# Kernel tuning notes

Measured on AMD Instinct MI355X. Metric: run time of the kernel, lower is better.

## Reference

```python
import jax, jax.numpy as jnp
import numpy as np

T, B, F, H, P = 256, 512, 256, 512, 12  # seq len, batch, feature_dim, hidden_dim, p_interval


def setup_inputs() -> dict:
    key = jax.random.key(0)
    ks = jax.random.split(key, 9)
    s = 1.0 / np.sqrt(F + H)  # torch Linear default init scale
    def lin(k):
        kw, kb = jax.random.split(k)
        W = jax.random.uniform(kw, (F + H, H), jnp.float32, -s, s)
        b = jax.random.uniform(kb, (H,), jnp.float32, -s, s)
        return W, b
    Wf, bf = lin(ks[0])
    Wi, bi = lin(ks[1])
    Wo, bo = lin(ks[2])
    Wg, bg = lin(ks[3])
    x = jax.random.normal(ks[4], (T, B, F), jnp.float32)
    return {"x": x, "Wf": Wf, "bf": bf, "Wi": Wi, "bi": bi,
            "Wo": Wo, "bo": bo, "Wg": Wg, "bg": bg}


def _slstm(x, Wf, bf, Wi, bi, Wo, bo, Wg, bg):
    Tn, Bn, _ = x.shape
    h0 = jnp.zeros((P, Bn, H), x.dtype)
    # NOTE: original torch code reassigns c to a 2D [B,H] tensor after step 0,
    # so c[t % P] indexes a batch ROW (shape [H]) that broadcasts. At t=0 the
    # slice is all-zeros either way, so carrying a 2D c is exactly faithful.
    c0 = jnp.zeros((Bn, H), x.dtype)

    def step(carry, inp):
        h, c = carry
        x_t, t = inp
        idx = t % P
        xc = jnp.concatenate([x_t, h[idx]], axis=1)  # [B, F+H]
        f = jax.nn.softmax(xc @ Wf + bf, axis=1)
        i = jax.nn.softmax(xc @ Wi + bi, axis=1)
        o = jax.nn.softmax(xc @ Wo + bo, axis=1)
        g = jnp.tanh(xc @ Wg + bg)
        c_new = jnp.tanh(f * c[idx] + i * g)  # c[idx]: row [H], broadcasts over B
        h = h.at[idx].set(o * c_new)
        return (h, c_new), None

    (h, _), _ = jax.lax.scan(step, (h0, c0), (x, jnp.arange(Tn)))
    return h[(Tn - 1) % P]


def reference(x, Wf, bf, Wi, bi, Wo, bo, Wg, bg):
    return _slstm(x, Wf, bf, Wi, bi, Wo, bo, Wg, bg)
```

## Files before the change

kernel.cpp:

```cpp
#include <hip/hip_runtime.h>

typedef unsigned short u16;
typedef unsigned int   u32;

typedef __attribute__((ext_vector_type(8))) short bf16x8;
typedef __attribute__((ext_vector_type(4))) float f32x4;

__device__ __forceinline__ u16 f2bf(float v) {
    u32 u = __float_as_uint(v);
    u32 r = (u + 0x7fffu + ((u >> 16) & 1u)) >> 16;
    return (u16)r;
}
__device__ __forceinline__ float bf2f(u16 h) { return __uint_as_float(((u32)h) << 16); }

__device__ __forceinline__ float ftanh(float x) {
    float e = __expf(2.0f * x);
    return 1.0f - 2.0f * __builtin_amdgcn_rcpf(e + 1.0f);
}

__device__ __forceinline__ void gl2lds16(const void* g, void* l) {
    __builtin_amdgcn_global_load_lds(
        (const __attribute__((address_space(1))) void*)g,
        (__attribute__((address_space(3))) void*)l, 16, 0, 0);
}

__global__ void init_k(u16* __restrict__ hh, u16* __restrict__ hl, float* __restrict__ cb) {
    int i = blockIdx.x * 256 + threadIdx.x;
    hh[i] = 0; hl[i] = 0;
    if (i < 2 * 512) cb[i] = 0.0f;
}

__global__ void pack_wq(const float* __restrict__ Wf, const float* __restrict__ bf_,
                        const float* __restrict__ Wi, const float* __restrict__ bi_,
                        const float* __restrict__ Wo, const float* __restrict__ bo_,
                        const float* __restrict__ Wg, const float* __restrict__ bg_,
                        u16* __restrict__ wq, float* __restrict__ bias4) {
    int idx = blockIdx.x * 256 + threadIdx.x;
    int n = idx / 768, k = idx - n * 768;
    int gate = n >> 9, col = n & 511;
    const float* W = (gate == 0) ? Wf : (gate == 1) ? Wi : (gate == 2) ? Wo : Wg;
    float v = W[k * 512 + col];
    u16 h = f2bf(v);
    u16 l = f2bf(v - bf2f(h));
    size_t base = (size_t)n * 2304;
    if (k < 256) {
        wq[base + k] = h; wq[base + 512 + k] = h; wq[base + 256 + k] = l;
    } else {
        int d = k - 256;
        wq[base + 768 + d] = h; wq[base + 1792 + d] = h; wq[base + 1280 + d] = l;
    }
    if (k == 0) {
        const float* bb = (gate == 0) ? bf_ : (gate == 1) ? bi_ : (gate == 2) ? bo_ : bg_;
        bias4[n] = bb[col];
    }
}

__global__ void split_x(const float* __restrict__ src, u16* __restrict__ oh, u16* __restrict__ ol) {
    int i = blockIdx.x * 256 + threadIdx.x;
    float4 v = ((const float4*)src)[i];
    u16 hx = f2bf(v.x), hy = f2bf(v.y), hz = f2bf(v.z), hw = f2bf(v.w);
    u16 lx = f2bf(v.x - bf2f(hx)), ly = f2bf(v.y - bf2f(hy));
    u16 lz = f2bf(v.z - bf2f(hz)), lw = f2bf(v.w - bf2f(hw));
    uint2 hv; hv.x = (u32)hx | ((u32)hy << 16); hv.y = (u32)hz | ((u32)hw << 16);
    uint2 lv; lv.x = (u32)lx | ((u32)ly << 16); lv.y = (u32)lz | ((u32)lw << 16);
    ((uint2*)oh)[i] = hv;
    ((uint2*)ol)[i] = lv;
}

#define KT 36
__global__ __launch_bounds__(512, 2) void gemm_q(
    const u16* __restrict__ xh, const u16* __restrict__ xl,
    const u16* __restrict__ hh, const u16* __restrict__ hl,
    const u16* __restrict__ wq, const float* __restrict__ bias4,
    float* __restrict__ lg, int gx) {
    __shared__ __align__(16) u16 smem[65536];

    const int tid = threadIdx.x;
    const int wid = tid >> 6, lane = tid & 63;
    const int l15 = lane & 15, l4 = lane >> 4;
    const int wm = wid >> 2, wn = wid & 3;

    const int xcd = blockIdx.x & 7, rr_ = blockIdx.x >> 3;
    const int bmp = gx >> 3;
    const int bm = xcd * bmp + (rr_ % bmp);
    const int bn = rr_ / bmp;

    u32 aox[2][2], aoh[2][2], adst[2][2];
    u32 boff[2][2], bdst[2][2];
#pragma unroll
    for (int q = 0; q < 2; ++q) {
        u32 idx = (u32)q * 512 + (u32)tid;
        u32 ro = idx >> 3, s = idx & 7, c = s ^ (ro & 7);
#pragma unroll
        for (int u = 0; u < 2; ++u) {
            u32 arow = (u32)bm * 256 + (ro & 63) + (ro >> 6) * 128 + (u32)u * 64;
            u32 alds = ((ro & 63) + (ro >> 6) * 128 + (u32)u * 64) * 64 + s * 8;
            aox[u][q] = arow * 256 + c * 8;
            aoh[u][q] = arow * 512 + c * 8;
            adst[u][q] = alds;
            u32 bcol = (u32)bn * 256 + (u32)u * 128 + ro;
            boff[u][q] = bcol * 2304 + c * 8;
            bdst[u][q] = 16384 + ((u32)u * 128 + ro) * 64 + s * 8;
        }
    }

    u32 rA[8], rB[4], sK[2];
#pragma unroll
    for (int f = 0; f < 8; ++f) rA[f] = (u32)(wm * 128 + f * 16 + l15) * 64;
#pragma unroll
    for (int f = 0; f < 4; ++f) rB[f] = 16384u + (u32)(wn * 64 + f * 16 + l15) * 64;
#pragma unroll
    for (int ks = 0; ks < 2; ++ks) sK[ks] = (u32)(((ks * 4 + l4) ^ (lane & 7)) * 8);

    f32x4 acc[8][4];
#pragma unroll
    for (int f = 0; f < 8; ++f)
#pragma unroll
        for (int j = 0; j < 4; ++j) { acc[f][j].x = 0.f; acc[f][j].y = 0.f; acc[f][j].z = 0.f; acc[f][j].w = 0.f; }

    bf16x8 aH[4], bF[4];

#define STAGE_B(u) do {                                                       \
        gl2lds16(bsr + boff[u][0], smem + nb32 + bdst[u][0]);                 \
        gl2lds16(bsr + boff[u][1], smem + nb32 + bdst[u][1]); } while (0)
#define STAGE_A(u) do {                                                       \
        gl2lds16(as_ + (xp ? aox[u][0] : aoh[u][0]) + ako, smem + nb32 + adst[u][0]); \
        gl2lds16(as_ + (xp ? aox[u][1] : aoh[u][1]) + ako, smem + nb32 + adst[u][1]); } while (0)
#define RD_A(h, ks) do {                                                      \
        aH[0] = *(const bf16x8*)(smem + cb32 + rA[(h)*4+0] + sK[ks]);         \
        aH[1] = *(const bf16x8*)(smem + cb32 + rA[(h)*4+1] + sK[ks]);         \
        aH[2] = *(const bf16x8*)(smem + cb32 + rA[(h)*4+2] + sK[ks]);         \
        aH[3] = *(const bf16x8*)(smem + cb32 + rA[(h)*4+3] + sK[ks]); } while (0)
#define RD_B(ks) do {                                                         \
        bF[0] = *(const bf16x8*)(smem + cb32 + rB[0] + sK[ks]);               \
        bF[1] = *(const bf16x8*)(smem + cb32 + rB[1] + sK[ks]);               \
        bF[2] = *(const bf16x8*)(smem + cb32 + rB[2] + sK[ks]);               \
        bF[3] = *(const bf16x8*)(smem + cb32 + rB[3] + sK[ks]); } while (0)
#define MM16(hb) do {                                                         \
        __builtin_amdgcn_s_setprio(1);                                        \
        _Pragma("unroll")                                                     \
        for (int fi_ = 0; fi_ < 4; ++fi_)                                     \
            _Pragma("unroll")                                                 \
            for (int fj_ = 0; fj_ < 4; ++fj_)                                 \
                acc[(hb)*4+fi_][fj_] = __builtin_amdgcn_mfma_f32_16x16x32_bf16(\
                    aH[fi_], bF[fj_], acc[(hb)*4+fi_][fj_], 0, 0, 0);         \
        __builtin_amdgcn_s_setprio(0);                                        \
    } while (0)
#define BAR() do { __builtin_amdgcn_s_barrier(); __builtin_amdgcn_sched_barrier(0); } while (0)

    {
        const int nb32 = 0;
        const u16* bsr = wq;
        const u16* as_ = xh; const u32 ako = 0; const bool xp = true;
        STAGE_B(0); STAGE_B(1); STAGE_A(0); STAGE_A(1);
    }
    asm volatile("s_waitcnt vmcnt(2)" ::: "memory");
    BAR();

#pragma unroll 2
    for (int kt = 0; kt < KT; ++kt) {
        const int cb32 = (kt & 1) << 15;
        const int nb32 = cb32 ^ 32768;
        const int kn = kt + 1;
        const bool stg = (kn < KT);
        const u16* as_ = xh; u32 ako = 0; bool xp = true;
        if (stg) {
            if (kn < 12) { as_ = (kn >= 8) ? xl : xh; ako = (u32)(kn & 3) * 64; xp = true; }
            else { int s2 = kn - 12; as_ = (s2 >= 16) ? hl : hh; ako = (u32)(s2 & 7) * 64; xp = false; }
        }
        const u16* bsr = wq + (size_t)kn * 64;

        if (stg) STAGE_B(0);
        RD_B(0); RD_A(0, 0);
        BAR();
        MM16(0);
        if (stg) asm volatile("s_waitcnt vmcnt(2)" ::: "memory");
        else     asm volatile("s_waitcnt vmcnt(0)" ::: "memory");
        BAR();
        if (stg) STAGE_B(1);
        RD_A(1, 0);
        BAR();
        MM16(1);
        BAR();
        if (stg) STAGE_A(0);
        RD_B(1); RD_A(0, 1);
        BAR();
        MM16(0);
        BAR();
        if (stg) STAGE_A(1);
        RD_A(1, 1);
        BAR();
        MM16(1);
        if (stg) asm volatile("s_waitcnt vmcnt(2)" ::: "memory");
        BAR();
    }
#undef STAGE_B
#undef STAGE_A
#undef RD_A
#undef RD_B
#undef MM16
#undef BAR

#pragma unroll
    for (int fj = 0; fj < 4; ++fj) {
        int n = bn * 256 + wn * 64 + fj * 16 + l15;
        float bv = bias4[n];
#pragma unroll
        for (int f = 0; f < 8; ++f) {
            int row = bm * 256 + wm * 128 + f * 16 + l4 * 4;
            lg[(size_t)(row + 0) * 2048 + n] = acc[f][fj].x + bv;
            lg[(size_t)(row + 1) * 2048 + n] = acc[f][fj].y + bv;
            lg[(size_t)(row + 2) * 2048 + n] = acc[f][fj].z + bv;
            lg[(size_t)(row + 3) * 2048 + n] = acc[f][fj].w + bv;
        }
    }
}

__device__ __forceinline__ void chain_step(const float* __restrict__ lg, int j, int lane, float r[8]) {
    int rowb = (j + 1) % 12;
    const float* base = lg + (size_t)(j * 512 + rowb) * 2048 + lane * 8;
    float f[8], iv[8], g[8];
#pragma unroll
    for (int u = 0; u < 8; ++u) { f[u] = base[u]; iv[u] = base[512 + u]; g[u] = base[1536 + u]; }
    float mf = -1e30f, mi = -1e30f;
#pragma unroll
    for (int u = 0; u < 8; ++u) { mf = fmaxf(mf, f[u]); mi = fmaxf(mi, iv[u]); }
#pragma unroll
    for (int o = 32; o; o >>= 1) { mf = fmaxf(mf, __shfl_xor(mf, o)); mi = fmaxf(mi, __shfl_xor(mi, o)); }
    float sf = 0.f, si = 0.f;
#pragma unroll
    for (int u = 0; u < 8; ++u) {
        f[u] = __expf(f[u] - mf); sf += f[u];
        iv[u] = __expf(iv[u] - mi); si += iv[u];
    }
#pragma unroll
    for (int o = 32; o; o >>= 1) { sf += __shfl_xor(sf, o); si += __shfl_xor(si, o); }
    float rf = __builtin_amdgcn_rcpf(sf), ri = __builtin_amdgcn_rcpf(si);
#pragma unroll
    for (int u = 0; u < 8; ++u) {
        float gg = ftanh(g[u]);
        r[u] = ftanh(f[u] * rf * r[u] + iv[u] * ri * gg);
    }
}

__global__ __launch_bounds__(256) void gates_k(
    const float* __restrict__ lg, float* __restrict__ cb,
    u16* __restrict__ hh, u16* __restrict__ hl,
    float* __restrict__ out, int t0, int S, int rd, int wr) {
    __shared__ float rsh[512];
    const int widx = threadIdx.x >> 6, lane = threadIdx.x & 63;
    const int s = (S - 1) - (blockIdx.x >> 7);
    const int b = (blockIdx.x & 127) * 4 + widx;
    const int t = t0 + s;

    if (widx == 0) {
        float r[8];
#pragma unroll
        for (int u = 0; u < 8; ++u) r[u] = cb[rd * 512 + lane * 8 + u];
        for (int j = 0; j < s; ++j) chain_step(lg, j, lane, r);
#pragma unroll
        for (int u = 0; u < 8; ++u) rsh[lane * 8 + u] = r[u];
        if ((int)blockIdx.x == 127 && t0 + S < 256) {
            chain_step(lg, S - 1, lane, r);
#pragma unroll
            for (int u = 0; u < 8; ++u) cb[wr * 512 + lane * 8 + u] = r[u];
        }
    }
    __syncthreads();

    const float* row = lg + (size_t)(s * 512 + b) * 2048 + lane * 8;
    float f[8], iv[8], ov[8], g[8];
#pragma unroll
    for (int u = 0; u < 8; ++u) {
        f[u] = row[u]; iv[u] = row[512 + u]; ov[u] = row[1024 + u]; g[u] = row[1536 + u];
    }
    float mf = -1e30f, mi = -1e30f, mo = -1e30f;
#pragma unroll
    for (int u = 0; u < 8; ++u) { mf = fmaxf(mf, f[u]); mi = fmaxf(mi, iv[u]); mo = fmaxf(mo, ov[u]); }
#pragma unroll
    for (int o = 32; o; o >>= 1) {
        mf = fmaxf(mf, __shfl_xor(mf, o));
        mi = fmaxf(mi, __shfl_xor(mi, o));
        mo = fmaxf(mo, __shfl_xor(mo, o));
    }
    float sf = 0.f, si = 0.f, so = 0.f;
#pragma unroll
    for (int u = 0; u < 8; ++u) {
        f[u] = __expf(f[u] - mf); sf += f[u];
        iv[u] = __expf(iv[u] - mi); si += iv[u];
        ov[u] = __expf(ov[u] - mo); so += ov[u];
    }
#pragma unroll
    for (int o = 32; o; o >>= 1) {
        sf += __shfl_xor(sf, o); si += __shfl_xor(si, o); so += __shfl_xor(so, o);
    }
    float rf = __builtin_amdgcn_rcpf(sf), ri = __builtin_amdgcn_rcpf(si), ro = __builtin_amdgcn_rcpf(so);
    float hout[8];
#pragma unroll
    for (int u = 0; u < 8; ++u) {
        float rr = rsh[lane * 8 + u];
        float gg = ftanh(g[u]);
        float cv = ftanh(f[u] * rf * rr + iv[u] * ri * gg);
        hout[u] = ov[u] * ro * cv;
    }
    u32 hhp[4], hlp[4];
#pragma unroll
    for (int u = 0; u < 4; ++u) {
        u16 h0 = f2bf(hout[2 * u]), h1 = f2bf(hout[2 * u + 1]);
        u16 l0 = f2bf(hout[2 * u] - bf2f(h0)), l1 = f2bf(hout[2 * u + 1] - bf2f(h1));
        hhp[u] = (u32)h0 | ((u32)h1 << 16);
        hlp[u] = (u32)l0 | ((u32)l1 << 16);
    }
    size_t hb = ((size_t)(s * 512 + b)) * 512 + lane * 8;
    *(uint4*)&hh[hb] = make_uint4(hhp[0], hhp[1], hhp[2], hhp[3]);
    *(uint4*)&hl[hb] = make_uint4(hlp[0], hlp[1], hlp[2], hlp[3]);
    if (t == 255) {
        float* op = out + (size_t)b * 512 + lane * 8;
#pragma unroll
        for (int u = 0; u < 8; ++u) op[u] = hout[u];
    }
}

extern "C" void kernel_launch(void* const* d_in, const int* in_sizes, int n_in,
                              void* d_out, int out_size, void* d_ws, size_t ws_size,
                              hipStream_t stream) {
    const float* x   = (const float*)d_in[0];
    const float* Wf  = (const float*)d_in[1];
    const float* bf_ = (const float*)d_in[2];
    const float* Wi  = (const float*)d_in[3];
    const float* bi_ = (const float*)d_in[4];
    const float* Wo  = (const float*)d_in[5];
    const float* bo_ = (const float*)d_in[6];
    const float* Wg  = (const float*)d_in[7];
    const float* bg_ = (const float*)d_in[8];
    float* out = (float*)d_out;

    char* p = (char*)d_ws;
    u16* xh  = (u16*)p; p += 134217728;
    u16* xl  = (u16*)p; p += 134217728;
    u16* wq  = (u16*)p; p += 9437184;
    u16* hh  = (u16*)p; p += 6291456;
    u16* hl  = (u16*)p; p += 6291456;
    float* bias4 = (float*)p; p += 8192;
    float* cb    = (float*)p; p += 4096;
    float* lg    = (float*)p; p += 50331648;

    init_k<<<12288, 256, 0, stream>>>(hh, hl, cb);
    pack_wq<<<6144, 256, 0, stream>>>(Wf, bf_, Wi, bi_, Wo, bo_, Wg, bg_, wq, bias4);
    split_x<<<32768, 256, 0, stream>>>(x, xh, xl);

    for (int blk = 0; blk < 22; ++blk) {
        int t0 = blk * 12;
        int S = (256 - t0 >= 12) ? 12 : (256 - t0);
        int M = S * 512;
        int gx = M / 256;
        gemm_q<<<gx * 8, 512, 0, stream>>>(
            xh + (size_t)t0 * 512 * 256, xl + (size_t)t0 * 512 * 256,
            hh, hl, wq, bias4, lg, gx);
        gates_k<<<S * 128, 256, 0, stream>>>(lg, cb, hh, hl, out, t0, S, blk & 1, (blk + 1) & 1);
    }
}
```

Baseline: 2.007 ms.

## Relax GEMM barrier scheduling, skip zero-h K tiles on first block, vectorize init

Splits the barrier macro so only barriers that publish staged LDS data keep a full sched_barrier(0). The others use a plain s_barrier, and staging loads get a partial sched_barrier mask, giving the compiler more freedom to interleave loads, LDS reads and MFMAs. On the first time block the hidden state is all zeros, so the GEMM stops after the 12 x-only K tiles, skipping the h contribution. The init kernel also writes zeros with 16-byte stores and fewer blocks. The looser scheduling constraints risk reordering hazards around LDS buffer reuse.

```diff
diff --git a/kernel.cpp b/kernel.cpp
--- a/kernel.cpp
+++ b/kernel.cpp
@@ -24,10 +24,11 @@
         (__attribute__((address_space(3))) void*)l, 16, 0, 0);
 }
 
-__global__ void init_k(u16* __restrict__ hh, u16* __restrict__ hl, float* __restrict__ cb) {
+__global__ void init_k(uint4* __restrict__ hh4, uint4* __restrict__ hl4, float4* __restrict__ cb4) {
     int i = blockIdx.x * 256 + threadIdx.x;
-    hh[i] = 0; hl[i] = 0;
-    if (i < 2 * 512) cb[i] = 0.0f;
+    uint4 z = make_uint4(0u, 0u, 0u, 0u);
+    hh4[i] = z; hl4[i] = z;
+    if (i < 256) cb4[i] = make_float4(0.f, 0.f, 0.f, 0.f);
 }
 
 __global__ void pack_wq(const float* __restrict__ Wf, const float* __restrict__ bf_,
@@ -67,12 +68,11 @@
     ((uint2*)ol)[i] = lv;
 }
 
-#define KT 36
 __global__ __launch_bounds__(512, 2) void gemm_q(
     const u16* __restrict__ xh, const u16* __restrict__ xl,
     const u16* __restrict__ hh, const u16* __restrict__ hl,
     const u16* __restrict__ wq, const float* __restrict__ bias4,
-    float* __restrict__ lg, int gx) {
+    float* __restrict__ lg, int gx, int ktEnd) {
     __shared__ __align__(16) u16 smem[65536];
 
     const int tid = threadIdx.x;
@@ -146,23 +146,27 @@
                     aH[fi_], bF[fj_], acc[(hb)*4+fi_][fj_], 0, 0, 0);         \
         __builtin_amdgcn_s_setprio(0);                                        \
     } while (0)
-#define BAR() do { __builtin_amdgcn_s_barrier(); __builtin_amdgcn_sched_barrier(0); } while (0)
+#define FBAR() __builtin_amdgcn_s_barrier()
+#define SBV() __builtin_amdgcn_sched_barrier(0x10E)
+#define PUBLISH(n) do {                                                       \
+        asm volatile("s_waitcnt vmcnt(" #n ")" ::: "memory");                 \
+        __builtin_amdgcn_s_barrier();                                         \
+        __builtin_amdgcn_sched_barrier(0); } while (0)
 
     {
         const int nb32 = 0;
         const u16* bsr = wq;
         const u16* as_ = xh; const u32 ako = 0; const bool xp = true;
-        STAGE_B(0); STAGE_B(1); STAGE_A(0); STAGE_A(1);
-    }
-    asm volatile("s_waitcnt vmcnt(2)" ::: "memory");
-    BAR();
+        STAGE_B(0); SBV(); STAGE_B(1); SBV(); STAGE_A(0); SBV(); STAGE_A(1); SBV();
+    }
+    PUBLISH(2);
 
 #pragma unroll 2
-    for (int kt = 0; kt < KT; ++kt) {
+    for (int kt = 0; kt < ktEnd; ++kt) {
         const int cb32 = (kt & 1) << 15;
         const int nb32 = cb32 ^ 32768;
         const int kn = kt + 1;
-        const bool stg = (kn < KT);
+        const bool stg = (kn < ktEnd);
         const u16* as_ = xh; u32 ako = 0; bool xp = true;
         if (stg) {
             if (kn < 12) { as_ = (kn >= 8) ? xl : xh; ako = (u32)(kn & 3) * 64; xp = true; }
@@ -170,36 +174,37 @@
         }
         const u16* bsr = wq + (size_t)kn * 64;
 
-        if (stg) STAGE_B(0);
+        if (stg) { STAGE_B(0); SBV(); }
         RD_B(0); RD_A(0, 0);
-        BAR();
+        FBAR();
         MM16(0);
-        if (stg) asm volatile("s_waitcnt vmcnt(2)" ::: "memory");
-        else     asm volatile("s_waitcnt vmcnt(0)" ::: "memory");
-        BAR();
-        if (stg) STAGE_B(1);
+        if (stg) PUBLISH(2);
+        else     PUBLISH(0);
+        if (stg) { STAGE_B(1); SBV(); }
         RD_A(1, 0);
-        BAR();
+        FBAR();
         MM16(1);
-        BAR();
-        if (stg) STAGE_A(0);
+        FBAR();
+        if (stg) { STAGE_A(0); SBV(); }
         RD_B(1); RD_A(0, 1);
-        BAR();
+        FBAR();
         MM16(0);
-        BAR();
-        if (stg) STAGE_A(1);
+        FBAR();
+        if (stg) { STAGE_A(1); SBV(); }
         RD_A(1, 1);
-        BAR();
+        FBAR();
         MM16(1);
-        if (stg) asm volatile("s_waitcnt vmcnt(2)" ::: "memory");
-        BAR();
+        if (stg) PUBLISH(2);
+        else { __builtin_amdgcn_s_barrier(); }
     }
 #undef STAGE_B
 #undef STAGE_A
 #undef RD_A
 #undef RD_B
 #undef MM16
-#undef BAR
+#undef FBAR
+#undef SBV
+#undef PUBLISH
 
 #pragma unroll
     for (int fj = 0; fj < 4; ++fj) {
@@ -345,7 +350,7 @@
     float* cb    = (float*)p; p += 4096;
     float* lg    = (float*)p; p += 50331648;
 
-    init_k<<<12288, 256, 0, stream>>>(hh, hl, cb);
+    init_k<<<3072, 256, 0, stream>>>((uint4*)hh, (uint4*)hl, (float4*)cb);
     pack_wq<<<6144, 256, 0, stream>>>(Wf, bf_, Wi, bi_, Wo, bo_, Wg, bg_, wq, bias4);
     split_x<<<32768, 256, 0, stream>>>(x, xh, xl);
 
@@ -354,9 +359,10 @@
         int S = (256 - t0 >= 12) ? 12 : (256 - t0);
         int M = S * 512;
         int gx = M / 256;
+        int ktEnd = (blk == 0) ? 12 : 36;
         gemm_q<<<gx * 8, 512, 0, stream>>>(
             xh + (size_t)t0 * 512 * 256, xl + (size_t)t0 * 512 * 256,
-            hh, hl, wq, bias4, lg, gx);
+            hh, hl, wq, bias4, lg, gx, ktEnd);
         gates_k<<<S * 128, 256, 0, stream>>>(lg, cb, hh, hl, out, t0, S, blk & 1, (blk + 1) & 1);
     }
 }
```

After: 2.103 ms. 1.05x slower.
